# Performance work log

Hardware: AMD Instinct MI355X
Metric: run time of the kernel (lower is better)

## Reference

```python
import jax, jax.numpy as jnp
import numpy as np

B, T, C, H = 2, 1024, 1024, 16
D = C // H                      # head_dim = 64
NG, BS = 64, 16                 # HBS groups / block_size (1024 = 64*16)
SQ = 32                         # sqrt_dim (1024 = 32*32)


def layer_norm(x, g, b, eps=1e-5):
    m = jnp.mean(x, axis=-1, keepdims=True)
    v = jnp.var(x, axis=-1, keepdims=True)
    return (x - m) * jax.lax.rsqrt(v + eps) * g + b


def hbs_proj(x, pre_g, pre_b, block_w, w_row, w_col, alpha, bias):
    # HierarchicalBlockShuffleLayer forward (dim=1024, no padding needed)
    xn = layer_norm(x, pre_g, pre_b)
    x_flat = xn.reshape(-1, C)
    # block mixing: per-group 16x16 matmul, then flip feature axis
    g = x_flat.reshape(-1, NG, BS)
    y_mixed = jnp.einsum('ngi,gij->ngj', g, block_w).reshape(-1, C)
    block_out = y_mixed[..., ::-1]
    # monarch branch: 32x32 grid, right-multiply W_col then W_row^T
    grid = x_flat.reshape(-1, SQ, SQ)
    z = jnp.einsum('nij,jc->nic', grid, w_col)
    z = jnp.einsum('nic,rc->nir', z, w_row).reshape(-1, C)
    out = block_out + alpha * z + bias
    return out.reshape(x.shape)


def setup_inputs() -> dict:
    key = jax.random.key(0)
    ks = jax.random.split(key, 12)
    inp = {
        'x': jax.random.normal(ks[0], (B, T, C), jnp.float32),
        'c_attn_w': jax.random.normal(ks[1], (3 * C, C), jnp.float32) * (1.0 / np.sqrt(C)),
        'c_attn_b': jnp.zeros((3 * C,), jnp.float32),
        'focus_gate': jnp.float32(0.0),
        'attn_norm_g': jnp.ones((D,), jnp.float32),
        'attn_norm_b': jnp.zeros((D,), jnp.float32),
        'out_norm_g': jnp.ones((C,), jnp.float32),
        'out_norm_b': jnp.zeros((C,), jnp.float32),
        'proj_pre_g': jnp.ones((C,), jnp.float32),
        'proj_pre_b': jnp.zeros((C,), jnp.float32),
        'proj_block_w': jax.random.normal(ks[2], (NG, BS, BS), jnp.float32) * 0.5 / np.sqrt(BS),
        'proj_w_row': jax.random.normal(ks[3], (SQ, SQ), jnp.float32) * 0.1 / np.sqrt(SQ),
        'proj_w_col': jax.random.normal(ks[4], (SQ, SQ), jnp.float32) * 0.1 / np.sqrt(SQ),
        'proj_alpha': jnp.float32(0.0),
        'proj_bias': jnp.zeros((C,), jnp.float32),
    }
    return inp


def reference(x, c_attn_w, c_attn_b, focus_gate, attn_norm_g, attn_norm_b,
              out_norm_g, out_norm_b, proj_pre_g, proj_pre_b, proj_block_w,
              proj_w_row, proj_w_col, proj_alpha, proj_bias):
    scale = 1.0 / np.sqrt(D)
    qkv = x @ c_attn_w.T + c_attn_b                      # [B,T,3C]
    q, k, v = jnp.split(qkv, 3, axis=2)
    # [B,H,T,D]
    q = q.reshape(B, T, H, D).transpose(0, 2, 1, 3)
    k = k.reshape(B, T, H, D).transpose(0, 2, 1, 3)
    v = v.reshape(B, T, H, D).transpose(0, 2, 1, 3)

    # --- causal linear attention branch (fp32) ---
    Qp = jax.nn.elu(q * scale) + 1.0
    Kp = jax.nn.elu(k * scale) + 1.0
    KV = jnp.einsum('bhtd,bhte->bhtde', Kp, v)           # [B,H,T,D,D]
    KV_cum = jnp.cumsum(KV, axis=2)
    K_cum = jnp.cumsum(Kp, axis=2)
    numer = jnp.einsum('bhtd,bhtde->bhte', Qp, KV_cum)
    denom = jnp.einsum('bhtd,bhtd->bht', Qp, K_cum)[..., None]
    y_lin = numer / (denom + 1e-4)                       # [B,H,T,D]
    y_lin = layer_norm(y_lin.transpose(0, 2, 1, 3), attn_norm_g, attn_norm_b)
    y_lin = y_lin.transpose(0, 2, 1, 3)

    # --- standard causal SDPA branch ---
    scores = jnp.einsum('bhqd,bhkd->bhqk', q, k) * scale
    causal = jnp.tril(jnp.ones((T, T), bool))
    scores = jnp.where(causal, scores, -jnp.inf)
    attn = jax.nn.softmax(scores, axis=-1)
    y_sharp = jnp.einsum('bhqk,bhkd->bhqd', attn, v)

    # --- gated combine + output projection ---
    alpha = jax.nn.sigmoid(focus_gate)
    y = alpha * y_sharp + (1.0 - alpha) * y_lin
    y = y.transpose(0, 2, 1, 3).reshape(B, T, C)
    y = layer_norm(y, out_norm_g, out_norm_b)
    return hbs_proj(y, proj_pre_g, proj_pre_b, proj_block_w,
                    proj_w_row, proj_w_col, proj_alpha, proj_bias)
```

## Files before the change

kernel.cpp:

```cpp
#include <hip/hip_runtime.h>
#include <math.h>

constexpr int T_ = 1024;
constexpr int C_ = 1024;
constexpr int H_ = 16;
constexpr int D_ = 64;
#define SCALE 0.125f

typedef unsigned short u16;
typedef __attribute__((ext_vector_type(8))) short short8;
typedef __attribute__((ext_vector_type(4))) float f32x4;

__device__ __forceinline__ float elu1(float x) { return x > 0.f ? x + 1.f : expf(x); }

__device__ __forceinline__ u16 f2bf(float f) {
    union { float f; unsigned u; } c; c.f = f;
    unsigned r = (c.u + 0x7fffu + ((c.u >> 16) & 1u)) >> 16;
    return (u16)r;
}
__device__ __forceinline__ float bf2f(u16 u) {
    union { unsigned u; float f; } c; c.u = (unsigned)u << 16;
    return c.f;
}

#define GLL16(g, l)                                                            \
    __builtin_amdgcn_global_load_lds(                                          \
        (const __attribute__((address_space(1))) void*)(g),                    \
        (__attribute__((address_space(3))) void*)(l), 16, 0, 0)

__global__ __launch_bounds__(256) void k0_prep(
    const float* __restrict__ x, const float* __restrict__ w,
    const float* __restrict__ wcol, const float* __restrict__ wrow,
    const float* __restrict__ palpha,
    u16* __restrict__ xbf, u16* __restrict__ wbf, float* __restrict__ Mg)
{
    const int b = blockIdx.x;
    const int tid = threadIdx.x;
    if (b < 2048) {
        int i = b * 256 + tid;
        float4 v = reinterpret_cast<const float4*>(x)[i];
        ushort4 o;
        o.x = f2bf(v.x); o.y = f2bf(v.y); o.z = f2bf(v.z); o.w = f2bf(v.w);
        reinterpret_cast<ushort4*>(xbf)[i] = o;
    } else if (b < 5120) {
        int i = (b - 2048) * 256 + tid;
        float4 v = reinterpret_cast<const float4*>(w)[i];
        ushort4 o;
        o.x = f2bf(v.x); o.y = f2bf(v.y); o.z = f2bf(v.z); o.w = f2bf(v.w);
        reinterpret_cast<ushort4*>(wbf)[i] = o;
    } else {
        const int j = tid >> 3, r0 = (tid & 7) << 2;
        const float al = palpha[0];
        float acc[4] = {0.f, 0.f, 0.f, 0.f};
        for (int c = 0; c < 32; c++) {
            float wc = wcol[(j << 5) + c];
#pragma unroll
            for (int q = 0; q < 4; q++) acc[q] += wc * wrow[((r0 + q) << 5) + c];
        }
        float4 o = {al * acc[0], al * acc[1], al * acc[2], al * acc[3]};
        *reinterpret_cast<float4*>(&Mg[(j << 5) + r0]) = o;
    }
}

__global__ __launch_bounds__(256) void k1_qkv(
    const u16* __restrict__ xbf, const u16* __restrict__ wbf,
    const float* __restrict__ bias,
    u16* __restrict__ qb, u16* __restrict__ kb, u16* __restrict__ vb,
    u16* __restrict__ vtb)
{
    __shared__ __align__(16) u16 As[128 * 32];
    __shared__ __align__(16) u16 Bs[128 * 32];
    const int tid = threadIdx.x;
    const int wave = tid >> 6, lane = tid & 63;
    const int quad = lane >> 4, l15 = lane & 15;
    const int m0 = blockIdx.y << 7, n0 = blockIdx.x << 7;
    const int wm = (wave >> 1) << 6, wn = (wave & 1) << 6;

    const int rowS = (wave << 5) + (lane >> 2);
    const int seg8 = (lane & 3) << 3;
    const u16* gA1 = xbf + (size_t)(m0 + rowS) * 1024 + seg8;
    const u16* gA2 = gA1 + (size_t)16 * 1024;
    const u16* gB1 = wbf + (size_t)(n0 + rowS) * 1024 + seg8;
    const u16* gB2 = gB1 + (size_t)16 * 1024;
    u16* lA1 = &As[(wave << 5) * 32];
    u16* lA2 = lA1 + 16 * 32;
    u16* lB1 = &Bs[(wave << 5) * 32];
    u16* lB2 = lB1 + 16 * 32;

    f32x4 zero4 = {0.f, 0.f, 0.f, 0.f};
    f32x4 acc[4][4];
#pragma unroll
    for (int i = 0; i < 4; i++)
#pragma unroll
        for (int j = 0; j < 4; j++) acc[i][j] = zero4;

    for (int k0 = 0; k0 < 1024; k0 += 32) {
        GLL16(gA1 + k0, lA1);
        GLL16(gA2 + k0, lA2);
        GLL16(gB1 + k0, lB1);
        GLL16(gB2 + k0, lB2);
        __syncthreads();
        short8 a[4], b[4];
#pragma unroll
        for (int mi = 0; mi < 4; mi++)
            a[mi] = *(const short8*)&As[(wm + mi * 16 + l15) * 32 + (quad << 3)];
#pragma unroll
        for (int ni = 0; ni < 4; ni++)
            b[ni] = *(const short8*)&Bs[(wn + ni * 16 + l15) * 32 + (quad << 3)];
#pragma unroll
        for (int mi = 0; mi < 4; mi++)
#pragma unroll
            for (int ni = 0; ni < 4; ni++)
                acc[mi][ni] = __builtin_amdgcn_mfma_f32_16x16x32_bf16(
                    a[mi], b[ni], acc[mi][ni], 0, 0, 0);
        __syncthreads();
    }
#pragma unroll
    for (int ni = 0; ni < 4; ni++) {
        int n_g = n0 + wn + ni * 16 + l15;
        int which = n_g >> 10;
        int h = (n_g >> 6) & 15;
        int d = n_g & 63;
        u16* dst = (which == 0) ? qb : (which == 1) ? kb : vb;
        float bz = bias[n_g];
#pragma unroll
        for (int mi = 0; mi < 4; mi++) {
            int m_base = m0 + wm + mi * 16 + (quad << 2);
            int bi = m_base >> 10, t_base = m_base & 1023;
            u16 o4[4];
#pragma unroll
            for (int reg = 0; reg < 4; reg++) {
                o4[reg] = f2bf(acc[mi][ni][reg] + bz);
                dst[((size_t)(bi * 16 + h) << 16) + ((size_t)(t_base + reg) << 6)
                    + d] = o4[reg];
            }
            if (which == 2) {
                *(uint2*)&vtb[(((size_t)((bi * 16 + h) << 6) + d) << 10) +
                              t_base] = *(uint2*)o4;
            }
        }
    }
}

__global__ __launch_bounds__(256) void k2a_chunkkv(
    const u16* __restrict__ kb, const u16* __restrict__ vb,
    float* __restrict__ Sg, float* __restrict__ svg)
{
    const int chunk = blockIdx.x, bh = blockIdx.y;
    const int t0 = chunk << 6;
    __shared__ float Ks[64][65];
    __shared__ float Vs[64][65];
    const int tid = threadIdx.x;
    const u16* kp = kb + (size_t)bh * T_ * D_;
    const u16* vp = vb + (size_t)bh * T_ * D_;
#pragma unroll
    for (int ii = 0; ii < 16; ii++) {
        int idx = tid + (ii << 8);
        int row = idx >> 6, col = idx & 63;
        Ks[row][col] = elu1(bf2f(kp[(size_t)(t0 + row) * D_ + col]) * SCALE);
        Vs[row][col] = bf2f(vp[(size_t)(t0 + row) * D_ + col]);
    }
    __syncthreads();
    const int tr = tid >> 4, tc = tid & 15;
    const int d0 = tr * 4, e0 = tc * 4;
    float acc[4][4] = {};
    for (int c = 0; c < 64; c++) {
        float a[4], b[4];
#pragma unroll
        for (int i = 0; i < 4; i++) a[i] = Ks[c][d0 + i];
#pragma unroll
        for (int j = 0; j < 4; j++) b[j] = Vs[c][e0 + j];
#pragma unroll
        for (int i = 0; i < 4; i++)
#pragma unroll
            for (int j = 0; j < 4; j++) acc[i][j] += a[i] * b[j];
    }
    float* so = Sg + ((size_t)bh * 16 + chunk) * 4096;
#pragma unroll
    for (int i = 0; i < 4; i++) {
        float4 o = {acc[i][0], acc[i][1], acc[i][2], acc[i][3]};
        *reinterpret_cast<float4*>(&so[(d0 + i) * 64 + e0]) = o;
    }
    if (tc == 0) {
#pragma unroll
        for (int i = 0; i < 4; i++) {
            float s = 0.f;
            for (int c = 0; c < 64; c++) s += Ks[c][d0 + i];
            svg[((size_t)bh * 16 + chunk) * 64 + d0 + i] = s;
        }
    }
}

__global__ __launch_bounds__(256) void k2s_scan(
    float* __restrict__ Sg, float* __restrict__ svg)
{
    int gid = blockIdx.x * 256 + threadIdx.x;
    if (gid < 131072) {
        int bh = gid >> 12, e = gid & 4095;
        float* base = Sg + ((size_t)bh << 16) + e;
        float v[16];
#pragma unroll
        for (int c = 0; c < 16; c++) v[c] = base[(size_t)c << 12];
        float run = 0.f;
#pragma unroll
        for (int c = 0; c < 16; c++) {
            base[(size_t)c << 12] = run;
            run += v[c];
        }
    } else if (gid < 131072 + 2048) {
        int g2 = gid - 131072;
        int bh = g2 >> 6, d = g2 & 63;
        float* base = svg + ((size_t)bh << 10) + d;
        float v[16];
#pragma unroll
        for (int c = 0; c < 16; c++) v[c] = base[c << 6];
        float run = 0.f;
#pragma unroll
        for (int c = 0; c < 16; c++) {
            base[c << 6] = run;
            run += v[c];
        }
    }
}

__global__ __launch_bounds__(256) void k2b_lin(
    const u16* __restrict__ qbp, const u16* __restrict__ kbp,
    const u16* __restrict__ vbp,
    const float* __restrict__ Sg, const float* __restrict__ svg,
    const float* __restrict__ ang, const float* __restrict__ anb,
    float* __restrict__ ylin)
{
    const int chunk = blockIdx.x, bh = blockIdx.y;
    const int t0 = chunk << 6;
    __shared__ __align__(16) float bufA[64][68];
    __shared__ float bufQ[64][65];
    __shared__ float bufK[64][65];
    __shared__ float svec[64];
    const int tid = threadIdx.x;
    const u16* qp = qbp + (size_t)bh * T_ * D_;
    const u16* kp = kbp + (size_t)bh * T_ * D_;
    const u16* vp = vbp + (size_t)bh * T_ * D_;
    const float* sp = Sg + (((size_t)bh * 16 + chunk) << 12);
#pragma unroll
    for (int u = 0; u < 4; u++) {
        int idx = (tid + (u << 8)) << 2;
        int dd = idx >> 6, e = idx & 63;
        *(float4*)&bufA[dd][e] = *(const float4*)&sp[idx];
    }
    if (tid < 64) svec[tid] = svg[(((size_t)bh * 16 + chunk) << 6) + tid];
#pragma unroll
    for (int ii = 0; ii < 16; ii++) {
        int idx = tid + (ii << 8);
        int row = idx >> 6, col = idx & 63;
        bufQ[col][row] = elu1(bf2f(qp[(size_t)(t0 + row) * D_ + col]) * SCALE);
    }
    __syncthreads();
    const int tr = tid >> 4, tc = tid & 15;
    const int r0 = tr * 4, c0 = tc * 4;
    float N[4][4] = {};
    float pden[4];
    for (int dd = 0; dd < 64; dd++) {
        float a[4], b[4];
#pragma unroll
        for (int i = 0; i < 4; i++) a[i] = bufQ[dd][r0 + i];
#pragma unroll
        for (int j = 0; j < 4; j++) b[j] = bufA[dd][c0 + j];
#pragma unroll
        for (int i = 0; i < 4; i++)
#pragma unroll
            for (int j = 0; j < 4; j++) N[i][j] += a[i] * b[j];
    }
#pragma unroll
    for (int i = 0; i < 4; i++) {
        float s = 0.f;
#pragma unroll
        for (int j = 0; j < 4; j++) s += bufQ[c0 + j][r0 + i] * svec[c0 + j];
        pden[i] = s;
    }
    __syncthreads();
#pragma unroll
    for (int ii = 0; ii < 16; ii++) {
        int idx = tid + (ii << 8);
        int row = idx >> 6, col = idx & 63;
        bufK[col][row] = elu1(bf2f(kp[(size_t)(t0 + row) * D_ + col]) * SCALE);
        bufA[row][col] = bf2f(vp[(size_t)(t0 + row) * D_ + col]);
    }
    __syncthreads();
    float sc[4][4] = {};
    for (int dd = 0; dd < 64; dd++) {
        float a[4], b[4];
#pragma unroll
        for (int i = 0; i < 4; i++) a[i] = bufQ[dd][r0 + i];
#pragma unroll
        for (int j = 0; j < 4; j++) b[j] = bufK[dd][c0 + j];
#pragma unroll
        for (int i = 0; i < 4; i++)
#pragma unroll
            for (int j = 0; j < 4; j++) sc[i][j] += a[i] * b[j];
    }
    __syncthreads();
#pragma unroll
    for (int i = 0; i < 4; i++) {
        float s = 0.f;
#pragma unroll
        for (int j = 0; j < 4; j++) {
            float pv = ((c0 + j) <= (r0 + i)) ? sc[i][j] : 0.f;
            bufQ[c0 + j][r0 + i] = pv;
            s += pv;
        }
        pden[i] += s;
    }
#pragma unroll
    for (int i = 0; i < 4; i++) {
#pragma unroll
        for (int off = 1; off < 16; off <<= 1)
            pden[i] += __shfl_xor(pden[i], off);
    }
    __syncthreads();
    for (int c = 0; c < 64; c++) {
        float a[4], b[4];
#pragma unroll
        for (int i = 0; i < 4; i++) a[i] = bufQ[c][r0 + i];
#pragma unroll
        for (int j = 0; j < 4; j++) b[j] = bufA[c][c0 + j];
#pragma unroll
        for (int i = 0; i < 4; i++)
#pragma unroll
            for (int j = 0; j < 4; j++) N[i][j] += a[i] * b[j];
    }
    float yv[4][4], s1[4], s2[4];
#pragma unroll
    for (int i = 0; i < 4; i++) {
        float inv = 1.f / (pden[i] + 1e-4f);
        s1[i] = 0.f; s2[i] = 0.f;
#pragma unroll
        for (int j = 0; j < 4; j++) {
            float t = N[i][j] * inv;
            yv[i][j] = t; s1[i] += t; s2[i] += t * t;
        }
    }
#pragma unroll
    for (int i = 0; i < 4; i++) {
#pragma unroll
        for (int off = 1; off < 16; off <<= 1) {
            s1[i] += __shfl_xor(s1[i], off);
            s2[i] += __shfl_xor(s2[i], off);
        }
    }
#pragma unroll
    for (int i = 0; i < 4; i++) {
        float mean = s1[i] * (1.f / 64.f);
        float var = s2[i] * (1.f / 64.f) - mean * mean;
        float rstd = rsqrtf(var + 1e-5f);
        float4 o;
        o.x = (yv[i][0] - mean) * rstd * ang[c0 + 0] + anb[c0 + 0];
        o.y = (yv[i][1] - mean) * rstd * ang[c0 + 1] + anb[c0 + 1];
        o.z = (yv[i][2] - mean) * rstd * ang[c0 + 2] + anb[c0 + 2];
        o.w = (yv[i][3] - mean) * rstd * ang[c0 + 3] + anb[c0 + 3];
        *reinterpret_cast<float4*>(
            &ylin[((size_t)bh * T_ + t0 + r0 + i) * D_ + c0]) = o;
    }
}

__global__ __launch_bounds__(256) void k3a_part(
    const u16* __restrict__ qbp, const u16* __restrict__ kbp,
    const u16* __restrict__ vtb,
    float* __restrict__ Op, float* __restrict__ ml)
{
    const int job = blockIdx.x, bh = blockIdx.y;
    const int qi = job >> 1, half = job & 1;
    const int n = qi + 1;
    const int csplit = n >> 1;
    const int kbeg = half ? csplit : 0;
    const int kend = half ? n : csplit;
    __shared__ __align__(16) u16 Qs[64][72];
    __shared__ __align__(16) u16 Ks[64][72];
    __shared__ __align__(16) u16 Vt[64][72];
    __shared__ __align__(16) u16 Pa[64][72];
    const int tid = threadIdx.x;
    const int wave = tid >> 6, lane = tid & 63;
    const int quad = lane >> 4, l15 = lane & 15;
    const f32x4 zero4 = {0.f, 0.f, 0.f, 0.f};

#pragma unroll
    for (int u = 0; u < 2; u++) {
        int idx = (tid + (u << 8)) << 3;
        int r = idx >> 6, c = idx & 63;
        *(uint4*)&Qs[r][c] = *(const uint4*)
            &qbp[((size_t)bh << 16) + ((size_t)((qi << 6) + r) << 6) + c];
    }
    __syncthreads();
    short8 bq[2];
    bq[0] = *(const short8*)&Qs[(wave << 4) + l15][(quad << 3)];
    bq[1] = *(const short8*)&Qs[(wave << 4) + l15][32 + (quad << 3)];
    f32x4 O[4];
#pragma unroll
    for (int dt = 0; dt < 4; dt++) O[dt] = zero4;
    float m_run = -INFINITY, l_run = 0.f;
    const int r_g = (qi << 6) + (wave << 4) + l15;

    for (int ki = kbeg; ki < kend; ki++) {
        __syncthreads();
#pragma unroll
        for (int u = 0; u < 2; u++) {
            int idx = (tid + (u << 8)) << 3;
            int r = idx >> 6, c = idx & 63;
            *(uint4*)&Ks[r][c] = *(const uint4*)
                &kbp[((size_t)bh << 16) + ((size_t)((ki << 6) + r) << 6) + c];
            *(uint4*)&Vt[r][c] = *(const uint4*)
                &vtb[((size_t)((bh << 6) + r) << 10) + (ki << 6) + c];
        }
        __syncthreads();
        f32x4 st[4];
#pragma unroll
        for (int ct = 0; ct < 4; ct++) st[ct] = zero4;
#pragma unroll
        for (int ks = 0; ks < 2; ks++) {
#pragma unroll
            for (int ct = 0; ct < 4; ct++) {
                short8 a = *(const short8*)
                    &Ks[(ct << 4) + l15][(ks << 5) + (quad << 3)];
                st[ct] = __builtin_amdgcn_mfma_f32_16x16x32_bf16(
                    a, bq[ks], st[ct], 0, 0, 0);
            }
        }
        float mloc = -INFINITY;
#pragma unroll
        for (int ct = 0; ct < 4; ct++)
#pragma unroll
            for (int reg = 0; reg < 4; reg++) {
                int c_g = (ki << 6) + (ct << 4) + (quad << 2) + reg;
                float s = st[ct][reg] * SCALE;
                if (c_g > r_g) s = -INFINITY;
                st[ct][reg] = s;
                mloc = fmaxf(mloc, s);
            }
        mloc = fmaxf(mloc, __shfl_xor(mloc, 16));
        mloc = fmaxf(mloc, __shfl_xor(mloc, 32));
        float mnew = fmaxf(m_run, mloc);
        float corr = __expf(m_run - mnew);
        m_run = mnew;
        float rsum = 0.f;
#pragma unroll
        for (int ct = 0; ct < 4; ct++) {
            u16 pk[4];
#pragma unroll
            for (int reg = 0; reg < 4; reg++) {
                float pv = __expf(st[ct][reg] - mnew);
                rsum += pv;
                pk[reg] = f2bf(pv);
            }
            unsigned lo = (unsigned)pk[0] | ((unsigned)pk[1] << 16);
            unsigned hi = (unsigned)pk[2] | ((unsigned)pk[3] << 16);
            uint2 pkv; pkv.x = lo; pkv.y = hi;
            *(uint2*)&Pa[(wave << 4) + l15][(ct << 4) + (quad << 2)] = pkv;
        }
        rsum += __shfl_xor(rsum, 16);
        rsum += __shfl_xor(rsum, 32);
        l_run = l_run * corr + rsum;
        float co[4];
#pragma unroll
        for (int reg = 0; reg < 4; reg++)
            co[reg] = __shfl(corr, ((lane >> 4) << 2) + reg);
#pragma unroll
        for (int dt = 0; dt < 4; dt++)
#pragma unroll
            for (int reg = 0; reg < 4; reg++) O[dt][reg] *= co[reg];
#pragma unroll
        for (int ks = 0; ks < 2; ks++) {
            short8 ap = *(const short8*)
                &Pa[(wave << 4) + l15][(ks << 5) + (quad << 3)];
#pragma unroll
            for (int dt = 0; dt < 4; dt++) {
                short8 bv = *(const short8*)
                    &Vt[(dt << 4) + l15][(ks << 5) + (quad << 3)];
                O[dt] = __builtin_amdgcn_mfma_f32_16x16x32_bf16(
                    ap, bv, O[dt], 0, 0, 0);
            }
        }
    }
    float* ob = Op + (((size_t)bh * 32 + job) << 12);
#pragma unroll
    for (int dt = 0; dt < 4; dt++)
#pragma unroll
        for (int reg = 0; reg < 4; reg++) {
            int r = (wave << 4) + (quad << 2) + reg;
            int d = (dt << 4) + l15;
            ob[(r << 6) + d] = O[dt][reg];
        }
    if (quad == 0) {
        int r = (wave << 4) + l15;
        float* mlb = ml + (((size_t)bh * 32 + job) << 7);
        mlb[r] = m_run;
        mlb[64 + r] = l_run;
    }
}

__global__ __launch_bounds__(256) void k3c_comb(
    const float* __restrict__ Op, const float* __restrict__ ml,
    const float* __restrict__ ylin, const float* __restrict__ fg,
    float* __restrict__ ycomb)
{
    const int qi = blockIdx.x, bh = blockIdx.y;
    const int bi = bh >> 4, h = bh & 15;
    __shared__ float sm[4][64];
    const int tid = threadIdx.x;
    const float al = 1.f / (1.f + __expf(-fg[0]));
    const size_t b0 = (((size_t)bh * 32 + (qi << 1)) << 7);
    if (tid < 64) {
        sm[0][tid] = ml[b0 + tid];
        sm[1][tid] = ml[b0 + 64 + tid];
        sm[2][tid] = ml[b0 + 128 + tid];
        sm[3][tid] = ml[b0 + 192 + tid];
    }
    __syncthreads();
    const float* o0 = Op + (((size_t)bh * 32 + (qi << 1)) << 12);
    const float* o1 = o0 + 4096;
#pragma unroll
    for (int u = 0; u < 4; u++) {
        int idx = tid + (u << 8);
        int r = idx >> 4, d4 = (idx & 15) << 2;
        float m0 = sm[0][r], l0 = sm[1][r];
        float m1 = sm[2][r], l1 = sm[3][r];
        float m = fmaxf(m0, m1);
        float w0 = (m0 == -INFINITY) ? 0.f : __expf(m0 - m);
        float w1 = __expf(m1 - m);
        float inv = al / (l0 * w0 + l1 * w1);
        float4 a = *(const float4*)&o0[(r << 6) + d4];
        float4 b = *(const float4*)&o1[(r << 6) + d4];
        int t = (qi << 6) + r;
        float4 yl = *(const float4*)&ylin[((((size_t)bh << 10) + t) << 6) + d4];
        float4 o;
        o.x = (a.x * w0 + b.x * w1) * inv + (1.f - al) * yl.x;
        o.y = (a.y * w0 + b.y * w1) * inv + (1.f - al) * yl.y;
        o.z = (a.z * w0 + b.z * w1) * inv + (1.f - al) * yl.z;
        o.w = (a.w * w0 + b.w * w1) * inv + (1.f - al) * yl.w;
        *(float4*)&ycomb[((((size_t)(bi << 10) + t)) << 10) + (h << 6) + d4] = o;
    }
}

__global__ __launch_bounds__(256) void k4_proj(
    const float* __restrict__ ycomb,
    const float* __restrict__ og, const float* __restrict__ ob,
    const float* __restrict__ pg, const float* __restrict__ pb,
    const float* __restrict__ bw, const float* __restrict__ Mg,
    const float* __restrict__ pbias, float* __restrict__ out)
{
    const int tok = blockIdx.x;
    __shared__ float xb[1024];
    __shared__ float red[8];
    const int tid = threadIdx.x;
    const int c0 = tid << 2;
    const float* yrow = ycomb + ((size_t)tok << 10);
    float4 v4 = *reinterpret_cast<const float4*>(yrow + c0);
    float v[4] = {v4.x, v4.y, v4.z, v4.w};
    float s1 = v[0] + v[1] + v[2] + v[3];
    float s2 = v[0]*v[0] + v[1]*v[1] + v[2]*v[2] + v[3]*v[3];
#pragma unroll
    for (int off = 1; off < 64; off <<= 1) {
        s1 += __shfl_xor(s1, off); s2 += __shfl_xor(s2, off);
    }
    if ((tid & 63) == 0) { red[(tid >> 6) * 2] = s1; red[(tid >> 6) * 2 + 1] = s2; }
    __syncthreads();
    s1 = red[0] + red[2] + red[4] + red[6];
    s2 = red[1] + red[3] + red[5] + red[7];
    __syncthreads();
    {
        float mean = s1 * (1.f / 1024.f);
        float var = s2 * (1.f / 1024.f) - mean * mean;
        float rstd = rsqrtf(var + 1e-5f);
#pragma unroll
        for (int q = 0; q < 4; q++)
            v[q] = (v[q] - mean) * rstd * og[c0 + q] + ob[c0 + q];
    }
    s1 = v[0] + v[1] + v[2] + v[3];
    s2 = v[0]*v[0] + v[1]*v[1] + v[2]*v[2] + v[3]*v[3];
#pragma unroll
    for (int off = 1; off < 64; off <<= 1) {
        s1 += __shfl_xor(s1, off); s2 += __shfl_xor(s2, off);
    }
    if ((tid & 63) == 0) { red[(tid >> 6) * 2] = s1; red[(tid >> 6) * 2 + 1] = s2; }
    __syncthreads();
    s1 = red[0] + red[2] + red[4] + red[6];
    s2 = red[1] + red[3] + red[5] + red[7];
    {
        float mean = s1 * (1.f / 1024.f);
        float var = s2 * (1.f / 1024.f) - mean * mean;
        float rstd = rsqrtf(var + 1e-5f);
#pragma unroll
        for (int q = 0; q < 4; q++)
            xb[c0 + q] = (v[q] - mean) * rstd * pg[c0 + q] + pb[c0 + q];
    }
    __syncthreads();
    const int g = tid >> 2;
    const int jb = (tid & 3) << 2;
    float acc[4] = {0.f, 0.f, 0.f, 0.f};
    {
        const float* xg = &xb[g << 4];
        const float* bwg = &bw[(g << 8) + jb];
        for (int i = 0; i < 16; i++) {
            float xv = xg[i];
            float4 wv = *reinterpret_cast<const float4*>(&bwg[i << 4]);
            acc[0] += xv * wv.x; acc[1] += xv * wv.y;
            acc[2] += xv * wv.z; acc[3] += xv * wv.w;
        }
    }
    const int C0 = ((63 - g) << 4) + 12 - jb;
    const int i2 = C0 >> 5, r0 = C0 & 31;
    float z2[4] = {0.f, 0.f, 0.f, 0.f};
    {
        const float* xg = &xb[i2 << 5];
        const float* mg = &Mg[r0];
        for (int j = 0; j < 32; j++) {
            float xv = xg[j];
            float4 mv = *reinterpret_cast<const float4*>(&mg[j << 5]);
            z2[0] += xv * mv.x; z2[1] += xv * mv.y;
            z2[2] += xv * mv.z; z2[3] += xv * mv.w;
        }
    }
    float4 bz = *reinterpret_cast<const float4*>(&pbias[C0]);
    float4 o;
    o.x = acc[3] + z2[0] + bz.x;
    o.y = acc[2] + z2[1] + bz.y;
    o.z = acc[1] + z2[2] + bz.z;
    o.w = acc[0] + z2[3] + bz.w;
    *reinterpret_cast<float4*>(&out[((size_t)tok << 10) + C0]) = o;
}

extern "C" void kernel_launch(void* const* d_in, const int* in_sizes, int n_in,
                              void* d_out, int out_size, void* d_ws, size_t ws_size,
                              hipStream_t stream) {
    const float* x   = (const float*)d_in[0];
    const float* w   = (const float*)d_in[1];
    const float* wb  = (const float*)d_in[2];
    const float* fg  = (const float*)d_in[3];
    const float* ang = (const float*)d_in[4];
    const float* anb = (const float*)d_in[5];
    const float* ong = (const float*)d_in[6];
    const float* onb = (const float*)d_in[7];
    const float* ppg = (const float*)d_in[8];
    const float* ppb = (const float*)d_in[9];
    const float* pbw = (const float*)d_in[10];
    const float* pwr = (const float*)d_in[11];
    const float* pwc = (const float*)d_in[12];
    const float* pal = (const float*)d_in[13];
    const float* pbi = (const float*)d_in[14];

    uint8_t* p = (uint8_t*)d_ws;
    u16* xbf = (u16*)p;  p += (size_t)2048 * 1024 * 2;
    u16* wbf = (u16*)p;  p += (size_t)3072 * 1024 * 2;
    u16* qb  = (u16*)p;  p += (size_t)32 * 1024 * 64 * 2;
    u16* kb  = (u16*)p;  p += (size_t)32 * 1024 * 64 * 2;
    u16* vb  = (u16*)p;  p += (size_t)32 * 1024 * 64 * 2;
    u16* vtb = (u16*)p;  p += (size_t)32 * 1024 * 64 * 2;
    float* ylin  = (float*)p;  p += (size_t)32 * 1024 * 64 * 4;
    float* ycomb = (float*)p;  p += (size_t)32 * 1024 * 64 * 4;
    float* Sg    = (float*)p;  p += (size_t)32 * 16 * 4096 * 4;
    float* svg   = (float*)p;  p += (size_t)32 * 16 * 64 * 4;
    float* Mg    = (float*)p;  p += (size_t)32 * 32 * 4;
    float* Op    = (float*)p;  p += (size_t)32 * 32 * 4096 * 4;
    float* ml    = (float*)p;  p += (size_t)32 * 32 * 128 * 4;
    float* out   = (float*)d_out;

    k0_prep<<<5121, 256, 0, stream>>>(x, w, pwc, pwr, pal, xbf, wbf, Mg);
    k1_qkv<<<dim3(24, 16), 256, 0, stream>>>(xbf, wbf, wb, qb, kb, vb, vtb);
    k2a_chunkkv<<<dim3(16, 32), 256, 0, stream>>>(kb, vb, Sg, svg);
    k2s_scan<<<521, 256, 0, stream>>>(Sg, svg);
    k2b_lin<<<dim3(16, 32), 256, 0, stream>>>(qb, kb, vb, Sg, svg, ang, anb, ylin);
    k3a_part<<<dim3(32, 32), 256, 0, stream>>>(qb, kb, vtb, Op, ml);
    k3c_comb<<<dim3(16, 32), 256, 0, stream>>>(Op, ml, ylin, fg, ycomb);
    k4_proj<<<2048, 256, 0, stream>>>(ycomb, ong, onb, ppg, ppb, pbw, Mg, pbi, out);
}
```

Measured before the change: 212.3 us.

## Merge chunk-KV and flash-attention partials into one launch; fold combine into projection

The linear-attention chunk KV kernel and the causal SDPA partial kernel become a single launch. Block index selects the role, and the attention jobs are ordered heaviest-first. The gated combine of the two split partials with the linear branch now runs inside the output projection kernel, so the ycomb intermediate buffer and two launches go away. The intent is to cut launch overhead and let the independent workloads fill the GPU together. The cost is a shared LDS footprint sized for the larger role, and the gather inside k4_proj has a strided access pattern across heads.

After: 211.5 us. Within noise of the previous version (-0.4%).

```diff
diff --git a/kernel.cpp b/kernel.cpp
--- a/kernel.cpp
+++ b/kernel.cpp
@@ -142,51 +142,186 @@
     }
 }
 
-__global__ __launch_bounds__(256) void k2a_chunkkv(
-    const u16* __restrict__ kb, const u16* __restrict__ vb,
-    float* __restrict__ Sg, float* __restrict__ svg)
+__global__ __launch_bounds__(256) void k23(
+    const u16* __restrict__ qbp, const u16* __restrict__ kbp,
+    const u16* __restrict__ vbp, const u16* __restrict__ vtb,
+    float* __restrict__ Sg, float* __restrict__ svg,
+    float* __restrict__ Op, float* __restrict__ ml)
 {
-    const int chunk = blockIdx.x, bh = blockIdx.y;
-    const int t0 = chunk << 6;
-    __shared__ float Ks[64][65];
-    __shared__ float Vs[64][65];
+    __shared__ __align__(16) u16 smem[4 * 64 * 72];
+    const int bh = blockIdx.y;
     const int tid = threadIdx.x;
-    const u16* kp = kb + (size_t)bh * T_ * D_;
-    const u16* vp = vb + (size_t)bh * T_ * D_;
-#pragma unroll
-    for (int ii = 0; ii < 16; ii++) {
-        int idx = tid + (ii << 8);
-        int row = idx >> 6, col = idx & 63;
-        Ks[row][col] = elu1(bf2f(kp[(size_t)(t0 + row) * D_ + col]) * SCALE);
-        Vs[row][col] = bf2f(vp[(size_t)(t0 + row) * D_ + col]);
-    }
-    __syncthreads();
-    const int tr = tid >> 4, tc = tid & 15;
-    const int d0 = tr * 4, e0 = tc * 4;
-    float acc[4][4] = {};
-    for (int c = 0; c < 64; c++) {
-        float a[4], b[4];
-#pragma unroll
-        for (int i = 0; i < 4; i++) a[i] = Ks[c][d0 + i];
-#pragma unroll
-        for (int j = 0; j < 4; j++) b[j] = Vs[c][e0 + j];
-#pragma unroll
-        for (int i = 0; i < 4; i++)
-#pragma unroll
-            for (int j = 0; j < 4; j++) acc[i][j] += a[i] * b[j];
-    }
-    float* so = Sg + ((size_t)bh * 16 + chunk) * 4096;
-#pragma unroll
-    for (int i = 0; i < 4; i++) {
-        float4 o = {acc[i][0], acc[i][1], acc[i][2], acc[i][3]};
-        *reinterpret_cast<float4*>(&so[(d0 + i) * 64 + e0]) = o;
-    }
-    if (tc == 0) {
+
+    if (blockIdx.x < 32) {
+        const int job = 31 - (int)blockIdx.x;
+        const int qi = job >> 1, half = job & 1;
+        const int n = qi + 1;
+        const int csplit = n >> 1;
+        const int kbeg = half ? csplit : 0;
+        const int kend = half ? n : csplit;
+        u16 (*Qs)[72] = (u16(*)[72])smem;
+        u16 (*Ks)[72] = (u16(*)[72])(smem + 4608);
+        u16 (*Vt)[72] = (u16(*)[72])(smem + 9216);
+        u16 (*Pa)[72] = (u16(*)[72])(smem + 13824);
+        const int wave = tid >> 6, lane = tid & 63;
+        const int quad = lane >> 4, l15 = lane & 15;
+        const f32x4 zero4 = {0.f, 0.f, 0.f, 0.f};
+
+#pragma unroll
+        for (int u = 0; u < 2; u++) {
+            int idx = (tid + (u << 8)) << 3;
+            int r = idx >> 6, c = idx & 63;
+            *(uint4*)&Qs[r][c] = *(const uint4*)
+                &qbp[((size_t)bh << 16) + ((size_t)((qi << 6) + r) << 6) + c];
+        }
+        __syncthreads();
+        short8 bq[2];
+        bq[0] = *(const short8*)&Qs[(wave << 4) + l15][(quad << 3)];
+        bq[1] = *(const short8*)&Qs[(wave << 4) + l15][32 + (quad << 3)];
+        f32x4 O[4];
+#pragma unroll
+        for (int dt = 0; dt < 4; dt++) O[dt] = zero4;
+        float m_run = -INFINITY, l_run = 0.f;
+        const int r_g = (qi << 6) + (wave << 4) + l15;
+
+        for (int ki = kbeg; ki < kend; ki++) {
+            __syncthreads();
+#pragma unroll
+            for (int u = 0; u < 2; u++) {
+                int idx = (tid + (u << 8)) << 3;
+                int r = idx >> 6, c = idx & 63;
+                *(uint4*)&Ks[r][c] = *(const uint4*)
+                    &kbp[((size_t)bh << 16) + ((size_t)((ki << 6) + r) << 6) + c];
+                *(uint4*)&Vt[r][c] = *(const uint4*)
+                    &vtb[((size_t)((bh << 6) + r) << 10) + (ki << 6) + c];
+            }
+            __syncthreads();
+            f32x4 st[4];
+#pragma unroll
+            for (int ct = 0; ct < 4; ct++) st[ct] = zero4;
+#pragma unroll
+            for (int ks = 0; ks < 2; ks++) {
+#pragma unroll
+                for (int ct = 0; ct < 4; ct++) {
+                    short8 a = *(const short8*)
+                        &Ks[(ct << 4) + l15][(ks << 5) + (quad << 3)];
+                    st[ct] = __builtin_amdgcn_mfma_f32_16x16x32_bf16(
+                        a, bq[ks], st[ct], 0, 0, 0);
+                }
+            }
+            float mloc = -INFINITY;
+#pragma unroll
+            for (int ct = 0; ct < 4; ct++)
+#pragma unroll
+                for (int reg = 0; reg < 4; reg++) {
+                    int c_g = (ki << 6) + (ct << 4) + (quad << 2) + reg;
+                    float s = st[ct][reg] * SCALE;
+                    if (c_g > r_g) s = -INFINITY;
+                    st[ct][reg] = s;
+                    mloc = fmaxf(mloc, s);
+                }
+            mloc = fmaxf(mloc, __shfl_xor(mloc, 16));
+            mloc = fmaxf(mloc, __shfl_xor(mloc, 32));
+            float mnew = fmaxf(m_run, mloc);
+            float corr = __expf(m_run - mnew);
+            m_run = mnew;
+            float rsum = 0.f;
+#pragma unroll
+            for (int ct = 0; ct < 4; ct++) {
+                u16 pk[4];
+#pragma unroll
+                for (int reg = 0; reg < 4; reg++) {
+                    float pv = __expf(st[ct][reg] - mnew);
+                    rsum += pv;
+                    pk[reg] = f2bf(pv);
+                }
+                unsigned lo = (unsigned)pk[0] | ((unsigned)pk[1] << 16);
+                unsigned hi = (unsigned)pk[2] | ((unsigned)pk[3] << 16);
+                uint2 pkv; pkv.x = lo; pkv.y = hi;
+                *(uint2*)&Pa[(wave << 4) + l15][(ct << 4) + (quad << 2)] = pkv;
+            }
+            rsum += __shfl_xor(rsum, 16);
+            rsum += __shfl_xor(rsum, 32);
+            l_run = l_run * corr + rsum;
+            float co[4];
+#pragma unroll
+            for (int reg = 0; reg < 4; reg++)
+                co[reg] = __shfl(corr, ((lane >> 4) << 2) + reg);
+#pragma unroll
+            for (int dt = 0; dt < 4; dt++)
+#pragma unroll
+                for (int reg = 0; reg < 4; reg++) O[dt][reg] *= co[reg];
+#pragma unroll
+            for (int ks = 0; ks < 2; ks++) {
+                short8 ap = *(const short8*)
+                    &Pa[(wave << 4) + l15][(ks << 5) + (quad << 3)];
+#pragma unroll
+                for (int dt = 0; dt < 4; dt++) {
+                    short8 bv = *(const short8*)
+                        &Vt[(dt << 4) + l15][(ks << 5) + (quad << 3)];
+                    O[dt] = __builtin_amdgcn_mfma_f32_16x16x32_bf16(
+                        ap, bv, O[dt], 0, 0, 0);
+                }
+            }
+        }
+        float* ob = Op + (((size_t)bh * 32 + job) << 12);
+#pragma unroll
+        for (int dt = 0; dt < 4; dt++)
+#pragma unroll
+            for (int reg = 0; reg < 4; reg++) {
+                int r = (wave << 4) + (quad << 2) + reg;
+                int d = (dt << 4) + l15;
+                ob[(r << 6) + d] = O[dt][reg];
+            }
+        if (quad == 0) {
+            int r = (wave << 4) + l15;
+            float* mlb = ml + (((size_t)bh * 32 + job) << 7);
+            mlb[r] = m_run;
+            mlb[64 + r] = l_run;
+        }
+    } else {
+        const int chunk = (int)blockIdx.x - 32;
+        const int t0 = chunk << 6;
+        float* Ksf = (float*)smem;
+        float* Vsf = Ksf + 64 * 65;
+        const u16* kp = kbp + (size_t)bh * T_ * D_;
+        const u16* vp = vbp + (size_t)bh * T_ * D_;
+#pragma unroll
+        for (int ii = 0; ii < 16; ii++) {
+            int idx = tid + (ii << 8);
+            int row = idx >> 6, col = idx & 63;
+            Ksf[row * 65 + col] =
+                elu1(bf2f(kp[(size_t)(t0 + row) * D_ + col]) * SCALE);
+            Vsf[row * 65 + col] = bf2f(vp[(size_t)(t0 + row) * D_ + col]);
+        }
+        __syncthreads();
+        const int tr = tid >> 4, tc = tid & 15;
+        const int d0 = tr * 4, e0 = tc * 4;
+        float acc[4][4] = {};
+        for (int c = 0; c < 64; c++) {
+            float a[4], b[4];
+#pragma unroll
+            for (int i = 0; i < 4; i++) a[i] = Ksf[c * 65 + d0 + i];
+#pragma unroll
+            for (int j = 0; j < 4; j++) b[j] = Vsf[c * 65 + e0 + j];
+#pragma unroll
+            for (int i = 0; i < 4; i++)
+#pragma unroll
+                for (int j = 0; j < 4; j++) acc[i][j] += a[i] * b[j];
+        }
+        float* so = Sg + ((size_t)bh * 16 + chunk) * 4096;
 #pragma unroll
         for (int i = 0; i < 4; i++) {
-            float s = 0.f;
-            for (int c = 0; c < 64; c++) s += Ks[c][d0 + i];
-            svg[((size_t)bh * 16 + chunk) * 64 + d0 + i] = s;
+            float4 o = {acc[i][0], acc[i][1], acc[i][2], acc[i][3]};
+            *reinterpret_cast<float4*>(&so[(d0 + i) * 64 + e0]) = o;
+        }
+        if (tc == 0) {
+#pragma unroll
+            for (int i = 0; i < 4; i++) {
+                float s = 0.f;
+                for (int c = 0; c < 64; c++) s += Ksf[c * 65 + d0 + i];
+                svg[((size_t)bh * 16 + chunk) * 64 + d0 + i] = s;
+            }
         }
     }
 }
@@ -362,197 +497,49 @@
     }
 }
 
-__global__ __launch_bounds__(256) void k3a_part(
-    const u16* __restrict__ qbp, const u16* __restrict__ kbp,
-    const u16* __restrict__ vtb,
-    float* __restrict__ Op, float* __restrict__ ml)
-{
-    const int job = blockIdx.x, bh = blockIdx.y;
-    const int qi = job >> 1, half = job & 1;
-    const int n = qi + 1;
-    const int csplit = n >> 1;
-    const int kbeg = half ? csplit : 0;
-    const int kend = half ? n : csplit;
-    __shared__ __align__(16) u16 Qs[64][72];
-    __shared__ __align__(16) u16 Ks[64][72];
-    __shared__ __align__(16) u16 Vt[64][72];
-    __shared__ __align__(16) u16 Pa[64][72];
-    const int tid = threadIdx.x;
-    const int wave = tid >> 6, lane = tid & 63;
-    const int quad = lane >> 4, l15 = lane & 15;
-    const f32x4 zero4 = {0.f, 0.f, 0.f, 0.f};
-
-#pragma unroll
-    for (int u = 0; u < 2; u++) {
-        int idx = (tid + (u << 8)) << 3;
-        int r = idx >> 6, c = idx & 63;
-        *(uint4*)&Qs[r][c] = *(const uint4*)
-            &qbp[((size_t)bh << 16) + ((size_t)((qi << 6) + r) << 6) + c];
-    }
-    __syncthreads();
-    short8 bq[2];
-    bq[0] = *(const short8*)&Qs[(wave << 4) + l15][(quad << 3)];
-    bq[1] = *(const short8*)&Qs[(wave << 4) + l15][32 + (quad << 3)];
-    f32x4 O[4];
-#pragma unroll
-    for (int dt = 0; dt < 4; dt++) O[dt] = zero4;
-    float m_run = -INFINITY, l_run = 0.f;
-    const int r_g = (qi << 6) + (wave << 4) + l15;
-
-    for (int ki = kbeg; ki < kend; ki++) {
-        __syncthreads();
-#pragma unroll
-        for (int u = 0; u < 2; u++) {
-            int idx = (tid + (u << 8)) << 3;
-            int r = idx >> 6, c = idx & 63;
-            *(uint4*)&Ks[r][c] = *(const uint4*)
-                &kbp[((size_t)bh << 16) + ((size_t)((ki << 6) + r) << 6) + c];
-            *(uint4*)&Vt[r][c] = *(const uint4*)
-                &vtb[((size_t)((bh << 6) + r) << 10) + (ki << 6) + c];
-        }
-        __syncthreads();
-        f32x4 st[4];
-#pragma unroll
-        for (int ct = 0; ct < 4; ct++) st[ct] = zero4;
-#pragma unroll
-        for (int ks = 0; ks < 2; ks++) {
-#pragma unroll
-            for (int ct = 0; ct < 4; ct++) {
-                short8 a = *(const short8*)
-                    &Ks[(ct << 4) + l15][(ks << 5) + (quad << 3)];
-                st[ct] = __builtin_amdgcn_mfma_f32_16x16x32_bf16(
-                    a, bq[ks], st[ct], 0, 0, 0);
-            }
-        }
-        float mloc = -INFINITY;
-#pragma unroll
-        for (int ct = 0; ct < 4; ct++)
-#pragma unroll
-            for (int reg = 0; reg < 4; reg++) {
-                int c_g = (ki << 6) + (ct << 4) + (quad << 2) + reg;
-                float s = st[ct][reg] * SCALE;
-                if (c_g > r_g) s = -INFINITY;
-                st[ct][reg] = s;
-                mloc = fmaxf(mloc, s);
-            }
-        mloc = fmaxf(mloc, __shfl_xor(mloc, 16));
-        mloc = fmaxf(mloc, __shfl_xor(mloc, 32));
-        float mnew = fmaxf(m_run, mloc);
-        float corr = __expf(m_run - mnew);
-        m_run = mnew;
-        float rsum = 0.f;
-#pragma unroll
-        for (int ct = 0; ct < 4; ct++) {
-            u16 pk[4];
-#pragma unroll
-            for (int reg = 0; reg < 4; reg++) {
-                float pv = __expf(st[ct][reg] - mnew);
-                rsum += pv;
-                pk[reg] = f2bf(pv);
-            }
-            unsigned lo = (unsigned)pk[0] | ((unsigned)pk[1] << 16);
-            unsigned hi = (unsigned)pk[2] | ((unsigned)pk[3] << 16);
-            uint2 pkv; pkv.x = lo; pkv.y = hi;
-            *(uint2*)&Pa[(wave << 4) + l15][(ct << 4) + (quad << 2)] = pkv;
-        }
-        rsum += __shfl_xor(rsum, 16);
-        rsum += __shfl_xor(rsum, 32);
-        l_run = l_run * corr + rsum;
-        float co[4];
-#pragma unroll
-        for (int reg = 0; reg < 4; reg++)
-            co[reg] = __shfl(corr, ((lane >> 4) << 2) + reg);
-#pragma unroll
-        for (int dt = 0; dt < 4; dt++)
-#pragma unroll
-            for (int reg = 0; reg < 4; reg++) O[dt][reg] *= co[reg];
-#pragma unroll
-        for (int ks = 0; ks < 2; ks++) {
-            short8 ap = *(const short8*)
-                &Pa[(wave << 4) + l15][(ks << 5) + (quad << 3)];
-#pragma unroll
-            for (int dt = 0; dt < 4; dt++) {
-                short8 bv = *(const short8*)
-                    &Vt[(dt << 4) + l15][(ks << 5) + (quad << 3)];
-                O[dt] = __builtin_amdgcn_mfma_f32_16x16x32_bf16(
-                    ap, bv, O[dt], 0, 0, 0);
-            }
-        }
-    }
-    float* ob = Op + (((size_t)bh * 32 + job) << 12);
-#pragma unroll
-    for (int dt = 0; dt < 4; dt++)
-#pragma unroll
-        for (int reg = 0; reg < 4; reg++) {
-            int r = (wave << 4) + (quad << 2) + reg;
-            int d = (dt << 4) + l15;
-            ob[(r << 6) + d] = O[dt][reg];
-        }
-    if (quad == 0) {
-        int r = (wave << 4) + l15;
-        float* mlb = ml + (((size_t)bh * 32 + job) << 7);
-        mlb[r] = m_run;
-        mlb[64 + r] = l_run;
-    }
-}
-
-__global__ __launch_bounds__(256) void k3c_comb(
+__global__ __launch_bounds__(256) void k4_proj(
     const float* __restrict__ Op, const float* __restrict__ ml,
     const float* __restrict__ ylin, const float* __restrict__ fg,
-    float* __restrict__ ycomb)
-{
-    const int qi = blockIdx.x, bh = blockIdx.y;
-    const int bi = bh >> 4, h = bh & 15;
-    __shared__ float sm[4][64];
-    const int tid = threadIdx.x;
-    const float al = 1.f / (1.f + __expf(-fg[0]));
-    const size_t b0 = (((size_t)bh * 32 + (qi << 1)) << 7);
-    if (tid < 64) {
-        sm[0][tid] = ml[b0 + tid];
-        sm[1][tid] = ml[b0 + 64 + tid];
-        sm[2][tid] = ml[b0 + 128 + tid];
-        sm[3][tid] = ml[b0 + 192 + tid];
-    }
-    __syncthreads();
-    const float* o0 = Op + (((size_t)bh * 32 + (qi << 1)) << 12);
-    const float* o1 = o0 + 4096;
-#pragma unroll
-    for (int u = 0; u < 4; u++) {
-        int idx = tid + (u << 8);
-        int r = idx >> 4, d4 = (idx & 15) << 2;
-        float m0 = sm[0][r], l0 = sm[1][r];
-        float m1 = sm[2][r], l1 = sm[3][r];
-        float m = fmaxf(m0, m1);
-        float w0 = (m0 == -INFINITY) ? 0.f : __expf(m0 - m);
-        float w1 = __expf(m1 - m);
-        float inv = al / (l0 * w0 + l1 * w1);
-        float4 a = *(const float4*)&o0[(r << 6) + d4];
-        float4 b = *(const float4*)&o1[(r << 6) + d4];
-        int t = (qi << 6) + r;
-        float4 yl = *(const float4*)&ylin[((((size_t)bh << 10) + t) << 6) + d4];
-        float4 o;
-        o.x = (a.x * w0 + b.x * w1) * inv + (1.f - al) * yl.x;
-        o.y = (a.y * w0 + b.y * w1) * inv + (1.f - al) * yl.y;
-        o.z = (a.z * w0 + b.z * w1) * inv + (1.f - al) * yl.z;
-        o.w = (a.w * w0 + b.w * w1) * inv + (1.f - al) * yl.w;
-        *(float4*)&ycomb[((((size_t)(bi << 10) + t)) << 10) + (h << 6) + d4] = o;
-    }
-}
-
-__global__ __launch_bounds__(256) void k4_proj(
-    const float* __restrict__ ycomb,
     const float* __restrict__ og, const float* __restrict__ ob,
     const float* __restrict__ pg, const float* __restrict__ pb,
     const float* __restrict__ bw, const float* __restrict__ Mg,
     const float* __restrict__ pbias, float* __restrict__ out)
 {
     const int tok = blockIdx.x;
+    const int bi = tok >> 10, t = tok & 1023;
+    const int qi = t >> 6, r = t & 63;
+    __shared__ float ybuf[1024];
     __shared__ float xb[1024];
     __shared__ float red[8];
     const int tid = threadIdx.x;
+    {
+        const float al = 1.f / (1.f + __expf(-fg[0]));
+        const int h = tid >> 4;
+        const int d4 = (tid & 15) << 2;
+        const int bh = (bi << 4) + h;
+        const size_t b0 = (((size_t)bh * 32 + (qi << 1)) << 7);
+        float m0 = ml[b0 + r], l0 = ml[b0 + 64 + r];
+        float m1 = ml[b0 + 128 + r], l1 = ml[b0 + 192 + r];
+        float m = fmaxf(m0, m1);
+        float w0 = (m0 == -INFINITY) ? 0.f : __expf(m0 - m);
+        float w1 = __expf(m1 - m);
+        float inv = al / (l0 * w0 + l1 * w1);
+        const float* o0 = Op + (((size_t)bh * 32 + (qi << 1)) << 12) + (r << 6);
+        const float* o1 = o0 + 4096;
+        float4 a = *(const float4*)&o0[d4];
+        float4 b = *(const float4*)&o1[d4];
+        float4 yl = *(const float4*)
+            &ylin[((((size_t)bh << 10) + t) << 6) + d4];
+        float4 o;
+        o.x = (a.x * w0 + b.x * w1) * inv + (1.f - al) * yl.x;
+        o.y = (a.y * w0 + b.y * w1) * inv + (1.f - al) * yl.y;
+        o.z = (a.z * w0 + b.z * w1) * inv + (1.f - al) * yl.z;
+        o.w = (a.w * w0 + b.w * w1) * inv + (1.f - al) * yl.w;
+        *(float4*)&ybuf[(h << 6) + d4] = o;
+    }
+    __syncthreads();
     const int c0 = tid << 2;
-    const float* yrow = ycomb + ((size_t)tok << 10);
-    float4 v4 = *reinterpret_cast<const float4*>(yrow + c0);
+    float4 v4 = *reinterpret_cast<const float4*>(&ybuf[c0]);
     float v[4] = {v4.x, v4.y, v4.z, v4.w};
     float s1 = v[0] + v[1] + v[2] + v[3];
     float s2 = v[0]*v[0] + v[1]*v[1] + v[2]*v[2] + v[3]*v[3];
@@ -654,7 +641,6 @@
     u16* vb  = (u16*)p;  p += (size_t)32 * 1024 * 64 * 2;
     u16* vtb = (u16*)p;  p += (size_t)32 * 1024 * 64 * 2;
     float* ylin  = (float*)p;  p += (size_t)32 * 1024 * 64 * 4;
-    float* ycomb = (float*)p;  p += (size_t)32 * 1024 * 64 * 4;
     float* Sg    = (float*)p;  p += (size_t)32 * 16 * 4096 * 4;
     float* svg   = (float*)p;  p += (size_t)32 * 16 * 64 * 4;
     float* Mg    = (float*)p;  p += (size_t)32 * 32 * 4;
@@ -664,10 +650,9 @@
 
     k0_prep<<<5121, 256, 0, stream>>>(x, w, pwc, pwr, pal, xbf, wbf, Mg);
     k1_qkv<<<dim3(24, 16), 256, 0, stream>>>(xbf, wbf, wb, qb, kb, vb, vtb);
-    k2a_chunkkv<<<dim3(16, 32), 256, 0, stream>>>(kb, vb, Sg, svg);
+    k23<<<dim3(48, 32), 256, 0, stream>>>(qb, kb, vb, vtb, Sg, svg, Op, ml);
     k2s_scan<<<521, 256, 0, stream>>>(Sg, svg);
     k2b_lin<<<dim3(16, 32), 256, 0, stream>>>(qb, kb, vb, Sg, svg, ang, anb, ylin);
-    k3a_part<<<dim3(32, 32), 256, 0, stream>>>(qb, kb, vtb, Op, ml);
-    k3c_comb<<<dim3(16, 32), 256, 0, stream>>>(Op, ml, ylin, fg, ycomb);
-    k4_proj<<<2048, 256, 0, stream>>>(ycomb, ong, onb, ppg, ppb, pbw, Mg, pbi, out);
-}
+    k4_proj<<<2048, 256, 0, stream>>>(Op, ml, ylin, fg, ong, onb, ppg, ppb,
+                                      pbw, Mg, pbi, out);
+}
```
